# Performance work log

Measured on AMD Instinct MI355X. Metric: run time of the kernel, lower is better.

## Reference

```python
import jax, jax.numpy as jnp
import numpy as np

B, P, G = 32, 19248, 32
NUM_CLASSES = 41          # 40 foreground + background (index 0)
POS_TH, NEG_TH = 0.5, 0.4
NEGPOS_RATIO = 3
BBOX_ALPHA = 1.5
CONF_ALPHA = 6.5
VAR_C, VAR_S = 0.1, 0.2   # SSD encoding variances


def point_form(b):
    # (cx,cy,w,h) -> (x1,y1,x2,y2)
    return jnp.concatenate([b[:, :2] - b[:, 2:] / 2, b[:, :2] + b[:, 2:] / 2], axis=-1)


def jaccard(a, b):
    # a: [G,4], b: [P,4] point-form -> IoU [G,P]
    lt = jnp.maximum(a[:, None, :2], b[None, :, :2])
    rb = jnp.minimum(a[:, None, 2:], b[None, :, 2:])
    wh = jnp.clip(rb - lt, 0.0)
    inter = wh[..., 0] * wh[..., 1]
    area_a = ((a[:, 2] - a[:, 0]) * (a[:, 3] - a[:, 1]))[:, None]
    area_b = ((b[:, 2] - b[:, 0]) * (b[:, 3] - b[:, 1]))[None, :]
    return inter / (area_a + area_b - inter)


def encode(matched, priors):
    # matched: [P,4] point-form gt, priors: [P,4] center-size
    g_cxcy = ((matched[:, :2] + matched[:, 2:]) / 2 - priors[:, :2]) / (VAR_C * priors[:, 2:])
    g_wh = jnp.log(jnp.clip((matched[:, 2:] - matched[:, :2]) / priors[:, 2:], 1e-8)) / VAR_S
    return jnp.concatenate([g_cxcy, g_wh], axis=-1)


def match_one(gt_box, gt_label, priors_pf, priors):
    ov = jaccard(gt_box, priors_pf)                     # [G,P]
    best_truth_ov = ov.max(axis=0)                      # [P]
    best_truth_idx = ov.argmax(axis=0)                  # [P]
    best_prior_idx = ov.argmax(axis=1)                  # [G]
    # force each gt to keep its best prior
    best_truth_ov = best_truth_ov.at[best_prior_idx].set(2.0)
    best_truth_idx = best_truth_idx.at[best_prior_idx].set(jnp.arange(G))
    matched = gt_box[best_truth_idx]                    # [P,4]
    conf = gt_label[best_truth_idx] + 1                 # background = 0
    conf = jnp.where(best_truth_ov < POS_TH, -1, conf)  # neutral band
    conf = jnp.where(best_truth_ov < NEG_TH, 0, conf)   # negatives
    return encode(matched, priors), conf


def smooth_l1(x, t):
    d = jnp.abs(x - t)
    return jnp.where(d < 1.0, 0.5 * d * d, d - 0.5)


def setup_inputs() -> dict:
    key = jax.random.key(0)
    ks = jax.random.split(key, 7)
    loc_data = jax.random.normal(ks[0], (B, P, 4), dtype=jnp.float32) * 0.5
    conf_data = jax.random.normal(ks[1], (B, P, NUM_CLASSES), dtype=jnp.float32)
    cxcy = jax.random.uniform(ks[2], (P, 2), minval=0.02, maxval=0.98)
    wh = jax.random.uniform(ks[3], (P, 2), minval=0.05, maxval=0.4)
    priors = jnp.concatenate([cxcy, wh], axis=-1)
    gc = jax.random.uniform(ks[4], (B, G, 2), minval=0.2, maxval=0.8)
    gwh = jax.random.uniform(ks[5], (B, G, 2), minval=0.05, maxval=0.4)
    gt_bboxes = jnp.clip(jnp.concatenate([gc - gwh / 2, gc + gwh / 2], axis=-1), 0.0, 1.0)
    gt_labels = jax.random.randint(ks[6], (B, G), 0, 40)
    return {"loc_data": loc_data, "conf_data": conf_data, "priors": priors,
            "gt_bboxes": gt_bboxes, "gt_labels": gt_labels}


def reference(loc_data, conf_data, priors, gt_bboxes, gt_labels):
    priors_pf = point_form(priors)
    loc_t, conf_t = jax.vmap(match_one, in_axes=(0, 0, None, None))(
        gt_bboxes, gt_labels, priors_pf, priors)        # [B,P,4], [B,P]
    loc_t = jax.lax.stop_gradient(loc_t)                # targets are constants
    pos = conf_t > 0                                    # [B,P]
    num_pos = jnp.maximum(pos.sum(), 1).astype(loc_data.dtype)

    # localization loss: mean over positives of per-prior smooth-L1 (summed over 4)
    box_l = smooth_l1(loc_data, loc_t).sum(-1)          # [B,P]
    loss_B = (box_l * pos).sum() / num_pos * BBOX_ALPHA

    # hard negative mining on background confidence loss
    lse = jax.nn.logsumexp(conf_data, axis=-1)          # [B,P]
    tgt = jnp.clip(conf_t, 0)
    picked = jnp.take_along_axis(conf_data, tgt[..., None], axis=-1).squeeze(-1)
    loss_c = lse - picked                               # CE per prior
    mined = jnp.where(pos | (conf_t < 0), 0.0, loss_c)  # zero out pos & neutral
    order = jnp.argsort(-mined, axis=1)
    rank = jnp.argsort(order, axis=1)                   # rank of each prior by loss
    num_neg = jnp.clip(NEGPOS_RATIO * pos.sum(axis=1), 0, P - 1)  # [B]
    neg = (rank < num_neg[:, None]) & (conf_t == 0)

    keep = (pos | neg).astype(loc_data.dtype)
    loss_C = (loss_c * keep).sum() / num_pos * CONF_ALPHA
    return loss_B + loss_C
```

## Files before the change

kernel.cpp:

```cpp
#include <hip/hip_runtime.h>

static constexpr int B = 32;
static constexpr int P = 19248;
static constexpr int G = 32;
static constexpr int C = 41;
static constexpr float POS_TH = 0.5f;
static constexpr float NEG_TH = 0.4f;

static constexpr int TM = 128;
static constexpr int PBM = (P + TM - 1) / TM;
static constexpr int NPART = 8;
static constexpr int PPART = P / NPART;
static constexpr int P4 = P / 4;

__device__ __forceinline__ float sl1(float d) {
    d = fabsf(d);
    return d < 1.0f ? 0.5f * d * d : d - 0.5f;
}

__global__ __launch_bounds__(1024) void k_match(
    const float* __restrict__ priors, const float* __restrict__ gt,
    unsigned long long* __restrict__ bp_part, int* __restrict__ done) {
    int part = blockIdx.x, b = blockIdx.y;
    if (part == 0 && b == 0 && threadIdx.x == 0) *done = 0;
    int lane = threadIdx.x & 63, wid = threadIdx.x >> 6;
    int pbase = part * PPART;
#pragma unroll
    for (int gsub = 0; gsub < 2; ++gsub) {
        int g = wid + gsub * 16;
        float4 gb = reinterpret_cast<const float4*>(gt)[b * G + g];
        float ga = (gb.z - gb.x) * (gb.w - gb.y);
        float best = -1.0f; int bidx = 0;
        for (int i = lane; i < PPART; i += 64) {
            int p = pbase + i;
            float4 pr = reinterpret_cast<const float4*>(priors)[p];
            float px1 = pr.x - pr.z * 0.5f, py1 = pr.y - pr.w * 0.5f;
            float px2 = pr.x + pr.z * 0.5f, py2 = pr.y + pr.w * 0.5f;
            float parea = (px2 - px1) * (py2 - py1);
            float lx = fmaxf(gb.x, px1), ly = fmaxf(gb.y, py1);
            float rx = fminf(gb.z, px2), ry = fminf(gb.w, py2);
            float w = fmaxf(rx - lx, 0.0f), h = fmaxf(ry - ly, 0.0f);
            float inter = w * h;
            float iou = inter / (ga + parea - inter);
            if (iou > best) { best = iou; bidx = p; }
        }
        unsigned long long pk =
            ((unsigned long long)__float_as_uint(best) << 32)
            | (unsigned)(0xFFFFFFFFu - (unsigned)bidx);
#pragma unroll
        for (int d = 32; d; d >>= 1) {
            unsigned long long o = __shfl_xor(pk, d);
            if (o > pk) pk = o;
        }
        if (lane == 0) bp_part[(part * B + b) * G + g] = pk;
    }
}

__global__ __launch_bounds__(TM) void k_main(
    const float* __restrict__ loc_data, const float* __restrict__ conf_data,
    const float* __restrict__ priors, const float* __restrict__ gt,
    const int* __restrict__ labels,
    const unsigned long long* __restrict__ bp_part,
    float* __restrict__ mined, float4* __restrict__ partial) {
    int b = blockIdx.y;
    int p0 = blockIdx.x * TM;
    int tid = threadIdx.x;
    int p = p0 + tid;
    int lane = tid & 63, wid = tid >> 6;
    __shared__ float sconf[TM * C];
    __shared__ int sforce[G];
    __shared__ float4 sg[G];
    __shared__ float sarea[G];
    if (tid < G) {
        unsigned long long mx = 0ull;
#pragma unroll
        for (int q = 0; q < NPART; ++q) {
            unsigned long long v = bp_part[(q * B + b) * G + tid];
            mx = v > mx ? v : mx;
        }
        sforce[tid] = (int)(0xFFFFFFFFu - (unsigned)mx);
        float4 g4 = reinterpret_cast<const float4*>(gt)[b * G + tid];
        sg[tid] = g4;
        sarea[tid] = (g4.z - g4.x) * (g4.w - g4.y);
    }
    int valid = min(TM, P - p0);
    size_t gbase = ((size_t)b * P + p0) * C;
    int tot4 = (valid * C) >> 2;
    const float4* g4p = reinterpret_cast<const float4*>(conf_data + gbase);
    float4* s4 = reinterpret_cast<float4*>(sconf);
#if defined(__has_builtin) && __has_builtin(__builtin_amdgcn_global_load_lds)
    typedef const __attribute__((address_space(1))) char* gas1_t;
    typedef __attribute__((address_space(3))) char* las3_t;
#define GL(j) { int i = tid + (j) * TM; if (i < tot4) \
    __builtin_amdgcn_global_load_lds((gas1_t)(g4p + i), (las3_t)(s4 + i), 16, 0, 0); }
    GL(0) GL(1) GL(2) GL(3) GL(4) GL(5) GL(6) GL(7) GL(8) GL(9) GL(10)
#undef GL
    asm volatile("s_waitcnt vmcnt(0)" ::: "memory");
    __syncthreads();
#else
    float4 r0, r1, r2, r3, r4, r5, r6, r7, r8, r9, r10;
#define LD(j, rj) { int i = tid + (j) * TM; if (i < tot4) rj = g4p[i]; }
#define ST(j, rj) { int i = tid + (j) * TM; if (i < tot4) s4[i] = rj; }
    LD(0, r0) LD(1, r1) LD(2, r2) LD(3, r3) LD(4, r4) LD(5, r5)
    LD(6, r6) LD(7, r7) LD(8, r8) LD(9, r9) LD(10, r10)
    ST(0, r0) ST(1, r1) ST(2, r2) ST(3, r3) ST(4, r4) ST(5, r5)
    ST(6, r6) ST(7, r7) ST(8, r8) ST(9, r9) ST(10, r10)
#undef LD
#undef ST
    __syncthreads();
#endif

    float my_box = 0.0f, my_posc = 0.0f; int my_pos = 0;
    if (p < P) {
        float4 pr = reinterpret_cast<const float4*>(priors)[p];
        float px1 = pr.x - pr.z * 0.5f, py1 = pr.y - pr.w * 0.5f;
        float px2 = pr.x + pr.z * 0.5f, py2 = pr.y + pr.w * 0.5f;
        float parea = (px2 - px1) * (py2 - py1);
        float ov = -1.0f; int bidx = 0;
#pragma unroll
        for (int g = 0; g < G; ++g) {
            float4 gb = sg[g];
            float lx = fmaxf(gb.x, px1), ly = fmaxf(gb.y, py1);
            float rx = fminf(gb.z, px2), ry = fminf(gb.w, py2);
            float w = fmaxf(rx - lx, 0.0f), h = fmaxf(ry - ly, 0.0f);
            float inter = w * h;
            float iou = inter / (sarea[g] + parea - inter);
            if (iou > ov) { ov = iou; bidx = g; }
        }
        int fidx = -1;
#pragma unroll
        for (int g = 0; g < G; ++g)
            if (p == sforce[g]) fidx = g;
        bool pos = false, neutral = false;
        int gidx = 0, cls = 0;
        float boxl = 0.0f;
        if (fidx >= 0)            { pos = true; gidx = fidx; }
        else if (ov >= POS_TH)    { pos = true; gidx = bidx; }
        else if (ov >= NEG_TH)    { neutral = true; }
        if (pos) {
            cls = labels[b * G + gidx] + 1;
            float4 gb = sg[gidx];
            float mcx = (gb.x + gb.z) * 0.5f, mcy = (gb.y + gb.w) * 0.5f;
            float tx = (mcx - pr.x) / (0.1f * pr.z);
            float ty = (mcy - pr.y) / (0.1f * pr.w);
            float tw = __logf(fmaxf((gb.z - gb.x) / pr.z, 1e-8f)) / 0.2f;
            float th = __logf(fmaxf((gb.w - gb.y) / pr.w, 1e-8f)) / 0.2f;
            float4 ld = reinterpret_cast<const float4*>(loc_data)[b * P + p];
            boxl = sl1(ld.x - tx) + sl1(ld.y - ty) + sl1(ld.z - tw) + sl1(ld.w - th);
        }
        const float* cv = &sconf[tid * C];
        float mx = cv[0];
#pragma unroll
        for (int c = 1; c < C; ++c) mx = fmaxf(mx, cv[c]);
        float se = 0.0f;
#pragma unroll
        for (int c = 0; c < C; ++c) se += __expf(cv[c] - mx);
        float lse = mx + __logf(se);
        float lc = lse - cv[cls];
        mined[(size_t)b * P + p] = (pos || neutral) ? 0.0f : lc;
        my_pos = pos ? 1 : 0;
        my_box = boxl;
        my_posc = pos ? lc : 0.0f;
    }

#pragma unroll
    for (int d = 32; d; d >>= 1) {
        my_box  += __shfl_xor(my_box, d);
        my_posc += __shfl_xor(my_posc, d);
        my_pos  += __shfl_xor(my_pos, d);
    }
    __shared__ float rb[2], rc[2]; __shared__ int rp[2];
    if (lane == 0) { rb[wid] = my_box; rc[wid] = my_posc; rp[wid] = my_pos; }
    __syncthreads();
    if (tid == 0) {
        partial[b * PBM + blockIdx.x] =
            make_float4(rb[0] + rb[1], rc[0] + rc[1], (float)(rp[0] + rp[1]), 0.0f);
    }
}

__global__ __launch_bounds__(1024) void k_topk(
    const float* __restrict__ mined, const float4* __restrict__ partial,
    float* __restrict__ neg_b, int* __restrict__ done,
    float* __restrict__ out) {
    int b = blockIdx.x;
    const float4* mb4 = reinterpret_cast<const float4*>(mined + (size_t)b * P);
    int tid = threadIdx.x;
    int lane = tid & 63, wid = tid >> 6;

    int cnt = 0;
    if (tid < PBM) cnt = (int)partial[b * PBM + tid].z;
#pragma unroll
    for (int d = 32; d; d >>= 1) cnt += __shfl_xor(cnt, d);
    __shared__ int ired[16];
    if (lane == 0) ired[wid] = cnt;
    __syncthreads();
    int np = 0;
#pragma unroll
    for (int w2 = 0; w2 < 16; ++w2) np += ired[w2];
    int k = 3 * np; if (k > P - 1) k = P - 1;

    float negval = 0.0f;
    if (k > 0) {
        __shared__ unsigned hist[2048];
        __shared__ unsigned sel[3];
        __shared__ unsigned wtot[16];
        if (tid == 0) { sel[0] = 0u; sel[1] = (unsigned)k; sel[2] = 0u; }
        const int shifts[3] = {21, 10, 0};
        const int widths[3] = {11, 11, 10};
#pragma unroll
        for (int level = 0; level < 3; ++level) {
            int shift = shifts[level];
            unsigned bmask = (1u << widths[level]) - 1u;
            hist[tid] = 0u; hist[tid + 1024] = 0u;
            __syncthreads();
            unsigned pref = sel[0];
            unsigned pmask = level ? (0xFFFFFFFFu << (shift + widths[level])) : 0u;
            for (int i = tid; i < P4; i += 1024) {
                float4 v4 = mb4[i];
                unsigned v;
                v = __float_as_uint(v4.x); if ((v & pmask) == pref) atomicAdd(&hist[(v >> shift) & bmask], 1u);
                v = __float_as_uint(v4.y); if ((v & pmask) == pref) atomicAdd(&hist[(v >> shift) & bmask], 1u);
                v = __float_as_uint(v4.z); if ((v & pmask) == pref) atomicAdd(&hist[(v >> shift) & bmask], 1u);
                v = __float_as_uint(v4.w); if ((v & pmask) == pref) atomicAdd(&hist[(v >> shift) & bmask], 1u);
            }
            __syncthreads();
            unsigned h0 = hist[2 * tid], h1 = hist[2 * tid + 1];
            unsigned x = h0 + h1;
#pragma unroll
            for (int d = 1; d < 64; d <<= 1) {
                unsigned t = __shfl_down(x, d);
                if (lane + d < 64) x += t;
            }
            if (lane == 0) wtot[wid] = x;
            __syncthreads();
            unsigned above = 0;
            for (int w2 = wid + 1; w2 < 16; ++w2) above += wtot[w2];
            unsigned sp = x + above;
            unsigned s2 = sp - h0 - h1;
            unsigned s1 = s2 + h1;
            unsigned want = sel[1];
            __syncthreads();
            if (s1 >= want && s2 < want) {
                sel[0] = pref | (((2u * (unsigned)tid + 1u) & bmask) << shift);
                sel[1] = want - s2;
                sel[2] += s2;
            } else if (sp >= want && s1 < want) {
                sel[0] = pref | (((2u * (unsigned)tid) & bmask) << shift);
                sel[1] = want - s1;
                sel[2] += s1;
            }
            __syncthreads();
        }
        unsigned vk = sel[0];
        unsigned cnt_gt = sel[2];
        float vkf = __uint_as_float(vk);
        float ssum = 0.0f;
        for (int i = tid; i < P4; i += 1024) {
            float4 v4 = mb4[i];
            if (__float_as_uint(v4.x) > vk) ssum += v4.x;
            if (__float_as_uint(v4.y) > vk) ssum += v4.y;
            if (__float_as_uint(v4.z) > vk) ssum += v4.z;
            if (__float_as_uint(v4.w) > vk) ssum += v4.w;
        }
#pragma unroll
        for (int d = 32; d; d >>= 1) ssum += __shfl_xor(ssum, d);
        __shared__ float rs[16];
        if (lane == 0) rs[wid] = ssum;
        __syncthreads();
        if (tid == 0) {
            float tot = 0.0f;
#pragma unroll
            for (int w2 = 0; w2 < 16; ++w2) tot += rs[w2];
            negval = tot + (float)(k - (int)cnt_gt) * vkf;
        }
    }

    __shared__ bool islast;
    if (tid == 0) {
        neg_b[b] = negval;
        __threadfence();
        int old = atomicAdd(done, 1);
        islast = (old == B - 1);
    }
    __syncthreads();
    if (!islast) return;
    __threadfence();

    float sbx = 0.0f, sc = 0.0f, sp2 = 0.0f, sn = 0.0f;
    for (int i = tid; i < B * PBM; i += 1024) {
        float4 v = partial[i];
        sbx += v.x; sc += v.y; sp2 += v.z;
    }
    if (tid < B) sn = neg_b[tid];
#pragma unroll
    for (int d = 32; d; d >>= 1) {
        sbx += __shfl_xor(sbx, d);
        sc  += __shfl_xor(sc, d);
        sp2 += __shfl_xor(sp2, d);
        sn  += __shfl_xor(sn, d);
    }
    __shared__ float fr[16][4];
    if (lane == 0) { fr[wid][0] = sbx; fr[wid][1] = sc; fr[wid][2] = sp2; fr[wid][3] = sn; }
    __syncthreads();
    if (tid == 0) {
        float tb = 0, tc = 0, tp = 0, tn = 0;
#pragma unroll
        for (int w2 = 0; w2 < 16; ++w2) {
            tb += fr[w2][0]; tc += fr[w2][1]; tp += fr[w2][2]; tn += fr[w2][3];
        }
        float npos = fmaxf(tp, 1.0f);
        out[0] = tb / npos * 1.5f + (tc + tn) / npos * 6.5f;
    }
}

extern "C" void kernel_launch(void* const* d_in, const int* in_sizes, int n_in,
                              void* d_out, int out_size, void* d_ws, size_t ws_size,
                              hipStream_t stream) {
    const float* loc    = (const float*)d_in[0];
    const float* conf   = (const float*)d_in[1];
    const float* priors = (const float*)d_in[2];
    const float* gt     = (const float*)d_in[3];
    const int*   labels = (const int*)d_in[4];
    float* out = (float*)d_out;

    char* w = (char*)d_ws;
    float4* partial = (float4*)w;                      w += sizeof(float4) * B * PBM;
    float* mined  = (float*)w;                         w += sizeof(float) * B * P;
    unsigned long long* bp_part = (unsigned long long*)w;
    w += sizeof(unsigned long long) * NPART * B * G;
    float* negb   = (float*)w;                         w += sizeof(float) * B;
    int*   done   = (int*)w;                           w += sizeof(int);

    k_match<<<dim3(NPART, B), 1024, 0, stream>>>(priors, gt, bp_part, done);
    k_main<<<dim3(PBM, B), TM, 0, stream>>>(loc, conf, priors, gt, labels,
                                            bp_part, mined, partial);
    k_topk<<<B, 1024, 0, stream>>>(mined, partial, negb, done, out);
}
```

Baseline: 82.67 us.

## Parallelize per-GT best-prior search across many small blocks and overlap reduction with loads

The per-GT argmax over priors moves from 8 partitions of 1024-thread blocks, each looping over thousands of priors, to 76 blocks of 256 threads per batch. Each thread handles one prior and the kernel reduces per wave with shuffles and a ballot. The main kernel now combines the per-block partials (76 per GT) while its async conf loads into LDS are still in flight, so the reduction latency hides behind the loads. The trade-offs are a larger intermediate buffer and a wider final reduction in k_main. Tie-breaking still prefers the lowest prior index via the ballot and packed key.

```diff
diff --git a/kernel.cpp b/kernel.cpp
--- a/kernel.cpp
+++ b/kernel.cpp
@@ -9,8 +9,8 @@
 
 static constexpr int TM = 128;
 static constexpr int PBM = (P + TM - 1) / TM;
-static constexpr int NPART = 8;
-static constexpr int PPART = P / NPART;
+static constexpr int NBLK = (P + 255) / 256;
+static constexpr int NBS = 80;
 static constexpr int P4 = P / 4;
 
 __device__ __forceinline__ float sl1(float d) {
@@ -18,41 +18,69 @@
     return d < 1.0f ? 0.5f * d * d : d - 0.5f;
 }
 
-__global__ __launch_bounds__(1024) void k_match(
+__device__ __forceinline__ unsigned long long umax64(unsigned long long a,
+                                                     unsigned long long b) {
+    return a > b ? a : b;
+}
+
+__global__ __launch_bounds__(256) void k_match(
     const float* __restrict__ priors, const float* __restrict__ gt,
-    unsigned long long* __restrict__ bp_part, int* __restrict__ done) {
-    int part = blockIdx.x, b = blockIdx.y;
-    if (part == 0 && b == 0 && threadIdx.x == 0) *done = 0;
-    int lane = threadIdx.x & 63, wid = threadIdx.x >> 6;
-    int pbase = part * PPART;
-#pragma unroll
-    for (int gsub = 0; gsub < 2; ++gsub) {
-        int g = wid + gsub * 16;
-        float4 gb = reinterpret_cast<const float4*>(gt)[b * G + g];
-        float ga = (gb.z - gb.x) * (gb.w - gb.y);
-        float best = -1.0f; int bidx = 0;
-        for (int i = lane; i < PPART; i += 64) {
-            int p = pbase + i;
-            float4 pr = reinterpret_cast<const float4*>(priors)[p];
-            float px1 = pr.x - pr.z * 0.5f, py1 = pr.y - pr.w * 0.5f;
-            float px2 = pr.x + pr.z * 0.5f, py2 = pr.y + pr.w * 0.5f;
-            float parea = (px2 - px1) * (py2 - py1);
+    unsigned long long* __restrict__ bp_blk, int* __restrict__ done) {
+    int bx = blockIdx.x, b = blockIdx.y;
+    int tid = threadIdx.x;
+    if (bx == 0 && b == 0 && tid == 0) *done = 0;
+    int lane = tid & 63, wid = tid >> 6;
+    int p0 = bx * 256;
+    int p = p0 + tid;
+    __shared__ float4 sg[G];
+    __shared__ float sarea[G];
+    __shared__ unsigned long long swave[G][4];
+    if (tid < G) {
+        float4 g4 = reinterpret_cast<const float4*>(gt)[b * G + tid];
+        sg[tid] = g4;
+        sarea[tid] = (g4.z - g4.x) * (g4.w - g4.y);
+    }
+    __syncthreads();
+
+    bool valid = (p < P);
+    float px1 = 0, py1 = 0, px2 = 0, py2 = 0, parea = 0;
+    if (valid) {
+        float4 pr = reinterpret_cast<const float4*>(priors)[p];
+        px1 = pr.x - pr.z * 0.5f; py1 = pr.y - pr.w * 0.5f;
+        px2 = pr.x + pr.z * 0.5f; py2 = pr.y + pr.w * 0.5f;
+        parea = (px2 - px1) * (py2 - py1);
+    }
+#pragma unroll
+    for (int g = 0; g < G; ++g) {
+        float iou = -1.0f;
+        if (valid) {
+            float4 gb = sg[g];
             float lx = fmaxf(gb.x, px1), ly = fmaxf(gb.y, py1);
             float rx = fminf(gb.z, px2), ry = fminf(gb.w, py2);
             float w = fmaxf(rx - lx, 0.0f), h = fmaxf(ry - ly, 0.0f);
             float inter = w * h;
-            float iou = inter / (ga + parea - inter);
-            if (iou > best) { best = iou; bidx = p; }
-        }
-        unsigned long long pk =
-            ((unsigned long long)__float_as_uint(best) << 32)
-            | (unsigned)(0xFFFFFFFFu - (unsigned)bidx);
-#pragma unroll
-        for (int d = 32; d; d >>= 1) {
-            unsigned long long o = __shfl_xor(pk, d);
-            if (o > pk) pk = o;
-        }
-        if (lane == 0) bp_part[(part * B + b) * G + g] = pk;
+            iou = inter / (sarea[g] + parea - inter);
+        }
+        float m = iou;
+#pragma unroll
+        for (int d = 32; d; d >>= 1) m = fmaxf(m, __shfl_xor(m, d));
+        unsigned long long mask = __ballot(iou == m);
+        if (lane == 0) {
+            unsigned long long pk = 0ull;
+            if (m >= 0.0f) {
+                int src = __ffsll((unsigned long long)mask) - 1;
+                int pw = p0 + wid * 64 + src;
+                pk = ((unsigned long long)__float_as_uint(m) << 32)
+                   | (unsigned)(0xFFFFFFFFu - (unsigned)pw);
+            }
+            swave[g][wid] = pk;
+        }
+    }
+    __syncthreads();
+    if (tid < G) {
+        unsigned long long mx = umax64(umax64(swave[tid][0], swave[tid][1]),
+                                       umax64(swave[tid][2], swave[tid][3]));
+        bp_blk[((size_t)b * G + tid) * NBS + bx] = mx;
     }
 }
 
@@ -60,7 +88,7 @@
     const float* __restrict__ loc_data, const float* __restrict__ conf_data,
     const float* __restrict__ priors, const float* __restrict__ gt,
     const int* __restrict__ labels,
-    const unsigned long long* __restrict__ bp_part,
+    const unsigned long long* __restrict__ bp_blk,
     float* __restrict__ mined, float4* __restrict__ partial) {
     int b = blockIdx.y;
     int p0 = blockIdx.x * TM;
@@ -71,18 +99,8 @@
     __shared__ int sforce[G];
     __shared__ float4 sg[G];
     __shared__ float sarea[G];
-    if (tid < G) {
-        unsigned long long mx = 0ull;
-#pragma unroll
-        for (int q = 0; q < NPART; ++q) {
-            unsigned long long v = bp_part[(q * B + b) * G + tid];
-            mx = v > mx ? v : mx;
-        }
-        sforce[tid] = (int)(0xFFFFFFFFu - (unsigned)mx);
-        float4 g4 = reinterpret_cast<const float4*>(gt)[b * G + tid];
-        sg[tid] = g4;
-        sarea[tid] = (g4.z - g4.x) * (g4.w - g4.y);
-    }
+    __shared__ unsigned long long spart[G][4];
+
     int valid = min(TM, P - p0);
     size_t gbase = ((size_t)b * P + p0) * C;
     int tot4 = (valid * C) >> 2;
@@ -95,20 +113,44 @@
     __builtin_amdgcn_global_load_lds((gas1_t)(g4p + i), (las3_t)(s4 + i), 16, 0, 0); }
     GL(0) GL(1) GL(2) GL(3) GL(4) GL(5) GL(6) GL(7) GL(8) GL(9) GL(10)
 #undef GL
-    asm volatile("s_waitcnt vmcnt(0)" ::: "memory");
-    __syncthreads();
 #else
     float4 r0, r1, r2, r3, r4, r5, r6, r7, r8, r9, r10;
 #define LD(j, rj) { int i = tid + (j) * TM; if (i < tot4) rj = g4p[i]; }
-#define ST(j, rj) { int i = tid + (j) * TM; if (i < tot4) s4[i] = rj; }
     LD(0, r0) LD(1, r1) LD(2, r2) LD(3, r3) LD(4, r4) LD(5, r5)
     LD(6, r6) LD(7, r7) LD(8, r8) LD(9, r9) LD(10, r10)
+#undef LD
+#endif
+
+    {
+        int g = tid >> 2, q = tid & 3;
+        const unsigned long long* row = bp_blk + ((size_t)b * G + g) * NBS;
+        unsigned long long mx = 0ull;
+#pragma unroll
+        for (int j = 0; j < 19; ++j) {
+            int i = q * 19 + j;
+            if (i < NBLK) mx = umax64(mx, row[i]);
+        }
+        spart[g][q] = mx;
+    }
+    float4 g4l;
+    if (tid < G) g4l = reinterpret_cast<const float4*>(gt)[b * G + tid];
+    __syncthreads();
+    if (tid < G) {
+        unsigned long long mx = umax64(umax64(spart[tid][0], spart[tid][1]),
+                                       umax64(spart[tid][2], spart[tid][3]));
+        sforce[tid] = (int)(0xFFFFFFFFu - (unsigned)mx);
+        sg[tid] = g4l;
+        sarea[tid] = (g4l.z - g4l.x) * (g4l.w - g4l.y);
+    }
+#if defined(__has_builtin) && __has_builtin(__builtin_amdgcn_global_load_lds)
+    asm volatile("s_waitcnt vmcnt(0)" ::: "memory");
+#else
+#define ST(j, rj) { int i = tid + (j) * TM; if (i < tot4) s4[i] = rj; }
     ST(0, r0) ST(1, r1) ST(2, r2) ST(3, r3) ST(4, r4) ST(5, r5)
     ST(6, r6) ST(7, r7) ST(8, r8) ST(9, r9) ST(10, r10)
-#undef LD
 #undef ST
-    __syncthreads();
 #endif
+    __syncthreads();
 
     float my_box = 0.0f, my_posc = 0.0f; int my_pos = 0;
     if (p < P) {
@@ -326,13 +368,13 @@
     char* w = (char*)d_ws;
     float4* partial = (float4*)w;                      w += sizeof(float4) * B * PBM;
     float* mined  = (float*)w;                         w += sizeof(float) * B * P;
-    unsigned long long* bp_part = (unsigned long long*)w;
-    w += sizeof(unsigned long long) * NPART * B * G;
+    unsigned long long* bp_blk = (unsigned long long*)w;
+    w += sizeof(unsigned long long) * (size_t)B * G * NBS;
     float* negb   = (float*)w;                         w += sizeof(float) * B;
     int*   done   = (int*)w;                           w += sizeof(int);
 
-    k_match<<<dim3(NPART, B), 1024, 0, stream>>>(priors, gt, bp_part, done);
+    k_match<<<dim3(NBLK, B), 256, 0, stream>>>(priors, gt, bp_blk, done);
     k_main<<<dim3(PBM, B), TM, 0, stream>>>(loc, conf, priors, gt, labels,
-                                            bp_part, mined, partial);
+                                            bp_blk, mined, partial);
     k_topk<<<B, 1024, 0, stream>>>(mined, partial, negb, done, out);
 }
```

Result: slower. 94.39 us (+14.2%).

## Overlap conf staging load with IoU matching and skip atomics for zero mined values

Applied to the files above, without the earlier changes.

The wait on the asynchronous global-to-LDS copy of confidence logits now comes after the IoU matching and box-loss computation, so the matching math runs while the loads are in flight. In the selection kernel, zero-valued mined losses (positives, neutrals) are counted in a register and added to histogram bin 0 once instead of each doing a shared-memory atomic. This cuts atomic contention on bin 0 but adds an extra reduction, barriers, and a serial update per level.

```diff
diff --git a/kernel.cpp b/kernel.cpp
--- a/kernel.cpp
+++ b/kernel.cpp
@@ -16,6 +16,11 @@
 __device__ __forceinline__ float sl1(float d) {
     d = fabsf(d);
     return d < 1.0f ? 0.5f * d * d : d - 0.5f;
+}
+
+__device__ __forceinline__ unsigned long long umax64(unsigned long long a,
+                                                     unsigned long long b) {
+    return a > b ? a : b;
 }
 
 __global__ __launch_bounds__(1024) void k_match(
@@ -71,18 +76,21 @@
     __shared__ int sforce[G];
     __shared__ float4 sg[G];
     __shared__ float sarea[G];
+
     if (tid < G) {
         unsigned long long mx = 0ull;
 #pragma unroll
         for (int q = 0; q < NPART; ++q) {
             unsigned long long v = bp_part[(q * B + b) * G + tid];
-            mx = v > mx ? v : mx;
+            mx = umax64(mx, v);
         }
         sforce[tid] = (int)(0xFFFFFFFFu - (unsigned)mx);
         float4 g4 = reinterpret_cast<const float4*>(gt)[b * G + tid];
         sg[tid] = g4;
         sarea[tid] = (g4.z - g4.x) * (g4.w - g4.y);
     }
+    __syncthreads();
+
     int valid = min(TM, P - p0);
     size_t gbase = ((size_t)b * P + p0) * C;
     int tot4 = (valid * C) >> 2;
@@ -95,22 +103,32 @@
     __builtin_amdgcn_global_load_lds((gas1_t)(g4p + i), (las3_t)(s4 + i), 16, 0, 0); }
     GL(0) GL(1) GL(2) GL(3) GL(4) GL(5) GL(6) GL(7) GL(8) GL(9) GL(10)
 #undef GL
-    asm volatile("s_waitcnt vmcnt(0)" ::: "memory");
-    __syncthreads();
+#define STAGE_WAIT asm volatile("s_waitcnt vmcnt(0)" ::: "memory")
 #else
     float4 r0, r1, r2, r3, r4, r5, r6, r7, r8, r9, r10;
 #define LD(j, rj) { int i = tid + (j) * TM; if (i < tot4) rj = g4p[i]; }
-#define ST(j, rj) { int i = tid + (j) * TM; if (i < tot4) s4[i] = rj; }
     LD(0, r0) LD(1, r1) LD(2, r2) LD(3, r3) LD(4, r4) LD(5, r5)
     LD(6, r6) LD(7, r7) LD(8, r8) LD(9, r9) LD(10, r10)
-    ST(0, r0) ST(1, r1) ST(2, r2) ST(3, r3) ST(4, r4) ST(5, r5)
-    ST(6, r6) ST(7, r7) ST(8, r8) ST(9, r9) ST(10, r10)
 #undef LD
-#undef ST
-    __syncthreads();
+#define STAGE_WAIT do { \
+    int i; \
+    i = tid + 0*TM;  if (i < tot4) s4[i] = r0; \
+    i = tid + 1*TM;  if (i < tot4) s4[i] = r1; \
+    i = tid + 2*TM;  if (i < tot4) s4[i] = r2; \
+    i = tid + 3*TM;  if (i < tot4) s4[i] = r3; \
+    i = tid + 4*TM;  if (i < tot4) s4[i] = r4; \
+    i = tid + 5*TM;  if (i < tot4) s4[i] = r5; \
+    i = tid + 6*TM;  if (i < tot4) s4[i] = r6; \
+    i = tid + 7*TM;  if (i < tot4) s4[i] = r7; \
+    i = tid + 8*TM;  if (i < tot4) s4[i] = r8; \
+    i = tid + 9*TM;  if (i < tot4) s4[i] = r9; \
+    i = tid + 10*TM; if (i < tot4) s4[i] = r10; \
+} while (0)
 #endif
 
     float my_box = 0.0f, my_posc = 0.0f; int my_pos = 0;
+    bool pos = false, neutral = false;
+    int cls = 0;
     if (p < P) {
         float4 pr = reinterpret_cast<const float4*>(priors)[p];
         float px1 = pr.x - pr.z * 0.5f, py1 = pr.y - pr.w * 0.5f;
@@ -131,9 +149,7 @@
 #pragma unroll
         for (int g = 0; g < G; ++g)
             if (p == sforce[g]) fidx = g;
-        bool pos = false, neutral = false;
-        int gidx = 0, cls = 0;
-        float boxl = 0.0f;
+        int gidx = 0;
         if (fidx >= 0)            { pos = true; gidx = fidx; }
         else if (ov >= POS_TH)    { pos = true; gidx = bidx; }
         else if (ov >= NEG_TH)    { neutral = true; }
@@ -146,8 +162,16 @@
             float tw = __logf(fmaxf((gb.z - gb.x) / pr.z, 1e-8f)) / 0.2f;
             float th = __logf(fmaxf((gb.w - gb.y) / pr.w, 1e-8f)) / 0.2f;
             float4 ld = reinterpret_cast<const float4*>(loc_data)[b * P + p];
-            boxl = sl1(ld.x - tx) + sl1(ld.y - ty) + sl1(ld.z - tw) + sl1(ld.w - th);
-        }
+            my_box = sl1(ld.x - tx) + sl1(ld.y - ty) + sl1(ld.z - tw) + sl1(ld.w - th);
+        }
+        my_pos = pos ? 1 : 0;
+    }
+
+    STAGE_WAIT;
+#undef STAGE_WAIT
+    __syncthreads();
+
+    if (p < P) {
         const float* cv = &sconf[tid * C];
         float mx = cv[0];
 #pragma unroll
@@ -158,8 +182,6 @@
         float lse = mx + __logf(se);
         float lc = lse - cv[cls];
         mined[(size_t)b * P + p] = (pos || neutral) ? 0.0f : lc;
-        my_pos = pos ? 1 : 0;
-        my_box = boxl;
         my_posc = pos ? lc : 0.0f;
     }
 
@@ -204,6 +226,7 @@
         __shared__ unsigned hist[2048];
         __shared__ unsigned sel[3];
         __shared__ unsigned wtot[16];
+        __shared__ unsigned zcs;
         if (tid == 0) { sel[0] = 0u; sel[1] = (unsigned)k; sel[2] = 0u; }
         const int shifts[3] = {21, 10, 0};
         const int widths[3] = {11, 11, 10};
@@ -215,14 +238,37 @@
             __syncthreads();
             unsigned pref = sel[0];
             unsigned pmask = level ? (0xFFFFFFFFu << (shift + widths[level])) : 0u;
+            unsigned zc = 0;
             for (int i = tid; i < P4; i += 1024) {
                 float4 v4 = mb4[i];
                 unsigned v;
-                v = __float_as_uint(v4.x); if ((v & pmask) == pref) atomicAdd(&hist[(v >> shift) & bmask], 1u);
-                v = __float_as_uint(v4.y); if ((v & pmask) == pref) atomicAdd(&hist[(v >> shift) & bmask], 1u);
-                v = __float_as_uint(v4.z); if ((v & pmask) == pref) atomicAdd(&hist[(v >> shift) & bmask], 1u);
-                v = __float_as_uint(v4.w); if ((v & pmask) == pref) atomicAdd(&hist[(v >> shift) & bmask], 1u);
+                v = __float_as_uint(v4.x);
+                if (v) { if ((v & pmask) == pref) atomicAdd(&hist[(v >> shift) & bmask], 1u); }
+                else ++zc;
+                v = __float_as_uint(v4.y);
+                if (v) { if ((v & pmask) == pref) atomicAdd(&hist[(v >> shift) & bmask], 1u); }
+                else ++zc;
+                v = __float_as_uint(v4.z);
+                if (v) { if ((v & pmask) == pref) atomicAdd(&hist[(v >> shift) & bmask], 1u); }
+                else ++zc;
+                v = __float_as_uint(v4.w);
+                if (v) { if ((v & pmask) == pref) atomicAdd(&hist[(v >> shift) & bmask], 1u); }
+                else ++zc;
             }
+            if (level == 0) {
+#pragma unroll
+                for (int d = 32; d; d >>= 1) zc += __shfl_xor(zc, d);
+                if (lane == 0) wtot[wid] = zc;
+                __syncthreads();
+                if (tid == 0) {
+                    unsigned t = 0;
+#pragma unroll
+                    for (int w2 = 0; w2 < 16; ++w2) t += wtot[w2];
+                    zcs = t;
+                }
+            }
+            __syncthreads();
+            if (tid == 0 && pref == 0u) hist[0] += zcs;
             __syncthreads();
             unsigned h0 = hist[2 * tid], h1 = hist[2 * tid + 1];
             unsigned x = h0 + h1;
```

New measurement: 82.15 us. About the same (-0.6%).
